# Performance work log

Hardware: AMD Instinct MI355X
Metric: run time of the kernel (lower is better)

Reference implementation:

```python
import jax, jax.numpy as jnp
import numpy as np

GAMMA = 1.0

def _rbf_mean(X, Y, gamma):
    x2 = jnp.sum(X * X, axis=1)  # [n]
    y2 = jnp.sum(Y * Y, axis=1)  # [m]
    d2 = x2[:, None] + y2[None, :] - 2.0 * (X @ Y.T)
    d2 = jnp.maximum(d2, 0.0)
    return jnp.mean(jnp.exp(-gamma * d2))

def setup_inputs() -> dict:
    key = jax.random.key(0)
    k1, k2 = jax.random.split(key)
    N = jax.random.normal(k1, (8192, 256), dtype=jnp.float32)
    R = jax.random.normal(k2, (8192, 256), dtype=jnp.float32)
    return {"N": N, "R": R}

def reference(N, R):
    xx = _rbf_mean(N, N, GAMMA)
    yy = _rbf_mean(R, R, GAMMA)
    xy = _rbf_mean(N, R, GAMMA)
    mmd = xx + yy - 2.0 * xy
    return jnp.sqrt(mmd)
```

## Files before the change

kernel.cpp:

```cpp
#include <hip/hip_runtime.h>
#include <math.h>

typedef float f32x4 __attribute__((ext_vector_type(4)));
typedef int   i32x4 __attribute__((ext_vector_type(4)));
typedef int   i32x8 __attribute__((ext_vector_type(8)));
typedef float f32x2 __attribute__((ext_vector_type(2)));

#define MTOT 16384
#define HALF 8192
#define KDIM 256
#define BM 256
#define NB (MTOT / BM)
#define NBLK (NB * (NB + 1) / 2)
#define NBLOCKS 256
#define TPX (NBLK / 8)

#define GLDS16(g, l) __builtin_amdgcn_global_load_lds(                      \
    (const __attribute__((address_space(1))) void*)(g),                     \
    (__attribute__((address_space(3))) void*)(l), 16, 0, 0)

#define BAR() do { asm volatile("" ::: "memory");                           \
  __builtin_amdgcn_s_barrier(); asm volatile("" ::: "memory"); } while (0)

__global__ __launch_bounds__(256) void convert_kernel(
    const float* __restrict__ Nmat, const float* __restrict__ Rmat,
    unsigned int* __restrict__ Z, float* __restrict__ x2,
    float* __restrict__ accum, unsigned int* __restrict__ counter) {
  if (blockIdx.x == 0 && threadIdx.x == 0) { *accum = 0.f; *counter = 0u; }
  const int lane = threadIdx.x & 63;
  const int wv = threadIdx.x >> 6;
  const int row = blockIdx.x * 4 + wv;
  const float* src = (row < HALF) ? (Nmat + (size_t)row * KDIM)
                                  : (Rmat + (size_t)(row - HALF) * KDIM);
  float4 v = *(const float4*)(src + lane * 4);
  int pk = __builtin_amdgcn_cvt_pk_fp8_f32(v.x, v.y, 0, false);
  pk = __builtin_amdgcn_cvt_pk_fp8_f32(v.z, v.w, pk, true);
  Z[(size_t)row * (KDIM / 4) + lane] = (unsigned int)pk;
  f32x2 d01 = __builtin_amdgcn_cvt_pk_f32_fp8(pk, false);
  f32x2 d23 = __builtin_amdgcn_cvt_pk_f32_fp8(pk, true);
  float sq = d01[0] * d01[0] + d01[1] * d01[1] + d23[0] * d23[0] + d23[1] * d23[1];
  #pragma unroll
  for (int off = 32; off; off >>= 1) sq += __shfl_down(sq, off);
  if (lane == 0) x2[row] = -0.5f * sq;
}

__device__ __forceinline__ void decode_tile(int t, int& bm, int& bn) {
  const int u = NBLK - 1 - t;
  int rr = (int)((sqrtf(8.0f * (float)u + 1.0f) - 1.0f) * 0.5f);
  while (rr * (rr + 1) / 2 > u) --rr;
  while ((rr + 1) * (rr + 2) / 2 <= u) ++rr;
  bm = NB - 1 - rr;
  bn = bm + (t - (bm * NB - bm * (bm - 1) / 2));
}

__global__ __launch_bounds__(512, 2) void mmd_gemm(
    const unsigned char* __restrict__ Z, const float* __restrict__ x2,
    float* __restrict__ accum, unsigned int* __restrict__ counter,
    float* __restrict__ out) {
  __shared__ __align__(16) unsigned char As[2 * 32768];
  __shared__ __align__(16) unsigned char Bs[2 * 32768];
  __shared__ __align__(16) float x2h[2][512];
  __shared__ __align__(16) float wsred[8];

  const int tid  = threadIdx.x;
  const int lane = tid & 63;
  const int wid  = tid >> 6;
  const int wm   = wid >> 2;
  const int wn   = wid & 3;

  const int lr = lane >> 3;
  const int ls = lane & 7;
  const int cofs = lr * KDIM + ((ls ^ lr) << 4);

  const int fr = lane & 15;
  const int fq = lane >> 4;
  const int key = fr & 7;
  const int slotL = ((2 * fq) ^ key) * 16;
  const int slotH = ((2 * fq + 1) ^ key) * 16;

  const int xcd = blockIdx.x & 7;
  const int lb  = blockIdx.x >> 3;
  const int niter = (lb < (TPX & 31)) ? (TPX / 32 + 1) : (TPX / 32);
  const int nslab = 2 * niter;

  f32x4 acc[8][4];
  float running = 0.f;

  auto STAGE = [&](int bmv, int bnv, int h, int buf) {
    const unsigned char* Ab = Z + (size_t)bmv * (BM * KDIM) + h * 128 + cofs;
    const unsigned char* Bb = Z + (size_t)bnv * (BM * KDIM) + h * 128 + cofs;
    unsigned char* Ad = As + buf * 32768;
    unsigned char* Bd = Bs + buf * 32768;
    #pragma unroll
    for (int tt = 0; tt < 4; ++tt) {
      int i = wid * 4 + tt;
      GLDS16(Ab + i * 2048, Ad + i * 1024);
      GLDS16(Bb + i * 2048, Bd + i * 1024);
    }
  };

  auto STAGEX2 = [&](int bmv, int bnv, int par) {
    GLDS16((const unsigned char*)(x2 + bmv * BM) + lane * 16,
           (unsigned char*)&x2h[par][0]);
    GLDS16((const unsigned char*)(x2 + bnv * BM) + lane * 16,
           (unsigned char*)&x2h[par][256]);
  };

  auto ACCINIT = [&](int par) {
    float xch[4];
    #pragma unroll
    for (int tn = 0; tn < 4; ++tn)
      xch[tn] = x2h[par][256 + wn * 64 + tn * 16 + fr];
    #pragma unroll
    for (int tm = 0; tm < 8; ++tm) {
      f32x4 xr = *(const f32x4*)&x2h[par][wm * 128 + tm * 16 + fq * 4];
      #pragma unroll
      for (int tn = 0; tn < 4; ++tn)
        #pragma unroll
        for (int v = 0; v < 4; ++v)
          acc[tm][tn][v] = xr[v] + xch[tn];
    }
  };

  int cbm, cbn;
  decode_tile(xcd * TPX + lb, cbm, cbn);
  int nbm = cbm, nbn = cbn;
  int cpar = 0;

  STAGEX2(cbm, cbn, 0);
  STAGE(cbm, cbn, 0, 0);
  STAGE(cbm, cbn, 1, 1);
  asm volatile("s_waitcnt vmcnt(16)" ::: "memory");
  ACCINIT(0);

  for (int j = 0; j < nslab; ++j) {
    const int bsel = j & 1;
    if (j + 1 >= nslab)      asm volatile("s_waitcnt vmcnt(0)" ::: "memory");
    else if (bsel == 0)      asm volatile("s_waitcnt vmcnt(8)" ::: "memory");
    else                     asm volatile("s_waitcnt vmcnt(10)" ::: "memory");
    BAR();

    {
      const unsigned char* A_s = As + bsel * 32768;
      const unsigned char* B_s = Bs + bsel * 32768;
      i32x8 bf[4];
      #pragma unroll
      for (int tn = 0; tn < 4; ++tn) {
        int row = wn * 64 + tn * 16 + fr;
        i32x4 lo = *(const i32x4*)(B_s + row * 128 + slotL);
        i32x4 hi = *(const i32x4*)(B_s + row * 128 + slotH);
        bf[tn] = __builtin_shufflevector(lo, hi, 0, 1, 2, 3, 4, 5, 6, 7);
      }
      #pragma unroll
      for (int tm = 0; tm < 8; ++tm) {
        int row = wm * 128 + tm * 16 + fr;
        i32x4 lo = *(const i32x4*)(A_s + row * 128 + slotL);
        i32x4 hi = *(const i32x4*)(A_s + row * 128 + slotH);
        i32x8 af = __builtin_shufflevector(lo, hi, 0, 1, 2, 3, 4, 5, 6, 7);
        #pragma unroll
        for (int tn = 0; tn < 4; ++tn)
          acc[tm][tn] = __builtin_amdgcn_mfma_scale_f32_16x16x128_f8f6f4(
              af, bf[tn], acc[tm][tn], 0, 0,
              0, 0x7F7F7F7F, 0, 0x7F7F7F7F);
      }
    }
    BAR();

    if (j + 2 < nslab) {
      if (bsel == 0) {
        decode_tile(xcd * TPX + lb + 32 * ((j >> 1) + 1), nbm, nbn);
        STAGEX2(nbm, nbn, cpar ^ 1);
        STAGE(nbm, nbn, 0, 0);
      } else {
        STAGE(nbm, nbn, 1, 1);
      }
    }

    if (bsel == 1) {
      float amax = -1e30f;
      #pragma unroll
      for (int tm = 0; tm < 8; ++tm)
        #pragma unroll
        for (int tn = 0; tn < 4; ++tn) {
          float m1 = fmaxf(fmaxf(acc[tm][tn][0], acc[tm][tn][1]), acc[tm][tn][2]);
          amax = fmaxf(fmaxf(amax, m1), acc[tm][tn][3]);
        }

      float partial = 0.f;
      if (__any(amax > -40.f)) {
        #pragma unroll
        for (int tm = 0; tm < 8; ++tm)
          #pragma unroll
          for (int tn = 0; tn < 4; ++tn)
            #pragma unroll
            for (int v = 0; v < 4; ++v) {
              float a = fminf(acc[tm][tn][v], 0.f);
              partial += exp2f(a * 2.885390082f);
            }
      }
      float wgt = ((cbm < NB / 2) == (cbn < NB / 2)) ? 1.f : -1.f;
      if (cbm != cbn) wgt *= 2.f;
      running += partial * wgt;

      if (j + 2 < nslab) {
        asm volatile("s_waitcnt vmcnt(16)" ::: "memory");
        cpar ^= 1;
        ACCINIT(cpar);
        cbm = nbm; cbn = nbn;
      }
    }
  }

  #pragma unroll
  for (int off = 32; off; off >>= 1) running += __shfl_down(running, off);
  if (lane == 0) wsred[wid] = running;
  __syncthreads();
  if (tid == 0) {
    float bs = 0.f;
    #pragma unroll
    for (int w = 0; w < 8; ++w) bs += wsred[w];
    atomicAdd(accum, bs);
    __threadfence();
    unsigned int old = atomicAdd(counter, 1u);
    if (old == NBLOCKS - 1) {
      float tot = atomicAdd(accum, 0.f);
      float mmd = tot / ((float)HALF * (float)HALF);
      out[0] = sqrtf(fmaxf(mmd, 0.f));
    }
  }
}

extern "C" void kernel_launch(void* const* d_in, const int* in_sizes, int n_in,
                              void* d_out, int out_size, void* d_ws, size_t ws_size,
                              hipStream_t stream) {
  const float* Nmat = (const float*)d_in[0];
  const float* Rmat = (const float*)d_in[1];
  float* out = (float*)d_out;

  char* ws = (char*)d_ws;
  unsigned char* Z = (unsigned char*)ws;
  float* x2        = (float*)(ws + (size_t)MTOT * KDIM);
  float* accum     = (float*)(ws + (size_t)MTOT * KDIM + (size_t)MTOT * 4);
  unsigned int* counter = (unsigned int*)(ws + (size_t)MTOT * KDIM + (size_t)MTOT * 4 + 4);

  convert_kernel<<<MTOT / 4, 256, 0, stream>>>(Nmat, Rmat, (unsigned int*)Z, x2,
                                               accum, counter);
  mmd_gemm<<<NBLOCKS, 512, 0, stream>>>(Z, x2, accum, counter, out);
}
```

Before: 126.0 us.

## Load B fragments directly into registers and preload all row norms to LDS

The B operand tiles are no longer staged through shared memory. Each wave loads its B fragments straight from global memory into double-buffered registers, which removes the Bs LDS buffers and their ds_read traffic. All 16K row norms are preloaded once into LDS, which replaces the per-tile x2 staging. The main loop is restructured to process both K halves per iteration with explicit waitcnt counts. The cost is higher register pressure and uncoalesced per-lane global loads for B, plus 64KB of LDS for the norms.

```diff
diff --git a/kernel.cpp b/kernel.cpp
--- a/kernel.cpp
+++ b/kernel.cpp
@@ -58,8 +58,7 @@
     float* __restrict__ accum, unsigned int* __restrict__ counter,
     float* __restrict__ out) {
   __shared__ __align__(16) unsigned char As[2 * 32768];
-  __shared__ __align__(16) unsigned char Bs[2 * 32768];
-  __shared__ __align__(16) float x2h[2][512];
+  __shared__ __align__(16) float x2l[MTOT];
   __shared__ __align__(16) float wsred[8];
 
   const int tid  = threadIdx.x;
@@ -81,39 +80,39 @@
   const int xcd = blockIdx.x & 7;
   const int lb  = blockIdx.x >> 3;
   const int niter = (lb < (TPX & 31)) ? (TPX / 32 + 1) : (TPX / 32);
-  const int nslab = 2 * niter;
 
   f32x4 acc[8][4];
+  i32x4 bfA[8], bfB[8];
   float running = 0.f;
 
-  auto STAGE = [&](int bmv, int bnv, int h, int buf) {
+  auto STAGEA = [&](int bmv, int h, int buf) {
     const unsigned char* Ab = Z + (size_t)bmv * (BM * KDIM) + h * 128 + cofs;
-    const unsigned char* Bb = Z + (size_t)bnv * (BM * KDIM) + h * 128 + cofs;
     unsigned char* Ad = As + buf * 32768;
-    unsigned char* Bd = Bs + buf * 32768;
     #pragma unroll
     for (int tt = 0; tt < 4; ++tt) {
       int i = wid * 4 + tt;
       GLDS16(Ab + i * 2048, Ad + i * 1024);
-      GLDS16(Bb + i * 2048, Bd + i * 1024);
-    }
-  };
-
-  auto STAGEX2 = [&](int bmv, int bnv, int par) {
-    GLDS16((const unsigned char*)(x2 + bmv * BM) + lane * 16,
-           (unsigned char*)&x2h[par][0]);
-    GLDS16((const unsigned char*)(x2 + bnv * BM) + lane * 16,
-           (unsigned char*)&x2h[par][256]);
-  };
-
-  auto ACCINIT = [&](int par) {
+    }
+  };
+
+  auto LOADB = [&](int bnv, int h, i32x4* dst) {
+    const unsigned char* base = Z + (size_t)bnv * (BM * KDIM)
+                                  + (size_t)(wn * 64 + fr) * KDIM + h * 128 + fq * 32;
+    #pragma unroll
+    for (int tn = 0; tn < 4; ++tn) {
+      dst[2 * tn]     = *(const i32x4*)(base + (size_t)tn * 16 * KDIM);
+      dst[2 * tn + 1] = *(const i32x4*)(base + (size_t)tn * 16 * KDIM + 16);
+    }
+  };
+
+  auto ACCINIT = [&](int bmv, int bnv) {
     float xch[4];
     #pragma unroll
     for (int tn = 0; tn < 4; ++tn)
-      xch[tn] = x2h[par][256 + wn * 64 + tn * 16 + fr];
+      xch[tn] = x2l[bnv * BM + wn * 64 + tn * 16 + fr];
     #pragma unroll
     for (int tm = 0; tm < 8; ++tm) {
-      f32x4 xr = *(const f32x4*)&x2h[par][wm * 128 + tm * 16 + fq * 4];
+      f32x4 xr = *(const f32x4*)&x2l[bmv * BM + wm * 128 + tm * 16 + fq * 4];
       #pragma unroll
       for (int tn = 0; tn < 4; ++tn)
         #pragma unroll
@@ -122,93 +121,88 @@
     }
   };
 
-  int cbm, cbn;
+  auto COMPUTE = [&](const unsigned char* A_s, const i32x4* bfr) {
+    i32x8 bf[4];
+    #pragma unroll
+    for (int tn = 0; tn < 4; ++tn)
+      bf[tn] = __builtin_shufflevector(bfr[2 * tn], bfr[2 * tn + 1],
+                                       0, 1, 2, 3, 4, 5, 6, 7);
+    #pragma unroll
+    for (int tm = 0; tm < 8; ++tm) {
+      int row = wm * 128 + tm * 16 + fr;
+      i32x4 lo = *(const i32x4*)(A_s + row * 128 + slotL);
+      i32x4 hi = *(const i32x4*)(A_s + row * 128 + slotH);
+      i32x8 af = __builtin_shufflevector(lo, hi, 0, 1, 2, 3, 4, 5, 6, 7);
+      #pragma unroll
+      for (int tn = 0; tn < 4; ++tn)
+        acc[tm][tn] = __builtin_amdgcn_mfma_scale_f32_16x16x128_f8f6f4(
+            af, bf[tn], acc[tm][tn], 0, 0,
+            0, 0x7F7F7F7F, 0, 0x7F7F7F7F);
+    }
+  };
+
+  int cbm, cbn, nbm, nbn;
   decode_tile(xcd * TPX + lb, cbm, cbn);
-  int nbm = cbm, nbn = cbn;
-  int cpar = 0;
-
-  STAGEX2(cbm, cbn, 0);
-  STAGE(cbm, cbn, 0, 0);
-  STAGE(cbm, cbn, 1, 1);
-  asm volatile("s_waitcnt vmcnt(16)" ::: "memory");
-  ACCINIT(0);
-
-  for (int j = 0; j < nslab; ++j) {
-    const int bsel = j & 1;
-    if (j + 1 >= nslab)      asm volatile("s_waitcnt vmcnt(0)" ::: "memory");
-    else if (bsel == 0)      asm volatile("s_waitcnt vmcnt(8)" ::: "memory");
-    else                     asm volatile("s_waitcnt vmcnt(10)" ::: "memory");
-    BAR();
-
-    {
-      const unsigned char* A_s = As + bsel * 32768;
-      const unsigned char* B_s = Bs + bsel * 32768;
-      i32x8 bf[4];
+
+  #pragma unroll
+  for (int t = 0; t < 8; ++t) {
+    int i = wid * 8 + t;
+    GLDS16((const unsigned char*)x2 + i * 1024 + (size_t)lane * 16,
+           (unsigned char*)x2l + i * 1024);
+  }
+  STAGEA(cbm, 0, 0);
+  LOADB(cbn, 0, bfA);
+  STAGEA(cbm, 1, 1);
+  LOADB(cbn, 1, bfB);
+  asm volatile("s_waitcnt vmcnt(24)" ::: "memory");
+  BAR();
+  ACCINIT(cbm, cbn);
+
+  for (int s = 0; s < niter; ++s) {
+    const bool haveNext = (s + 1 < niter);
+    if (haveNext) decode_tile(xcd * TPX + lb + 32 * (s + 1), nbm, nbn);
+
+    asm volatile("s_waitcnt vmcnt(12)" ::: "memory");
+    BAR();
+    COMPUTE(As, bfA);
+    if (haveNext) LOADB(nbn, 0, bfA);
+    BAR();
+    if (haveNext) STAGEA(nbm, 0, 0);
+
+    if (haveNext) asm volatile("s_waitcnt vmcnt(12)" ::: "memory");
+    else          asm volatile("s_waitcnt vmcnt(0)"  ::: "memory");
+    BAR();
+    COMPUTE(As + 32768, bfB);
+    if (haveNext) LOADB(nbn, 1, bfB);
+    BAR();
+    if (haveNext) STAGEA(nbm, 1, 1);
+
+    float amax = -1e30f;
+    #pragma unroll
+    for (int tm = 0; tm < 8; ++tm)
       #pragma unroll
       for (int tn = 0; tn < 4; ++tn) {
-        int row = wn * 64 + tn * 16 + fr;
-        i32x4 lo = *(const i32x4*)(B_s + row * 128 + slotL);
-        i32x4 hi = *(const i32x4*)(B_s + row * 128 + slotH);
-        bf[tn] = __builtin_shufflevector(lo, hi, 0, 1, 2, 3, 4, 5, 6, 7);
+        float m1 = fmaxf(fmaxf(acc[tm][tn][0], acc[tm][tn][1]), acc[tm][tn][2]);
+        amax = fmaxf(fmaxf(amax, m1), acc[tm][tn][3]);
       }
-      #pragma unroll
-      for (int tm = 0; tm < 8; ++tm) {
-        int row = wm * 128 + tm * 16 + fr;
-        i32x4 lo = *(const i32x4*)(A_s + row * 128 + slotL);
-        i32x4 hi = *(const i32x4*)(A_s + row * 128 + slotH);
-        i32x8 af = __builtin_shufflevector(lo, hi, 0, 1, 2, 3, 4, 5, 6, 7);
+
+    float partial = 0.f;
+    if (__any(amax > -40.f)) {
+      #pragma unroll
+      for (int tm = 0; tm < 8; ++tm)
         #pragma unroll
         for (int tn = 0; tn < 4; ++tn)
-          acc[tm][tn] = __builtin_amdgcn_mfma_scale_f32_16x16x128_f8f6f4(
-              af, bf[tn], acc[tm][tn], 0, 0,
-              0, 0x7F7F7F7F, 0, 0x7F7F7F7F);
-      }
-    }
-    BAR();
-
-    if (j + 2 < nslab) {
-      if (bsel == 0) {
-        decode_tile(xcd * TPX + lb + 32 * ((j >> 1) + 1), nbm, nbn);
-        STAGEX2(nbm, nbn, cpar ^ 1);
-        STAGE(nbm, nbn, 0, 0);
-      } else {
-        STAGE(nbm, nbn, 1, 1);
-      }
-    }
-
-    if (bsel == 1) {
-      float amax = -1e30f;
-      #pragma unroll
-      for (int tm = 0; tm < 8; ++tm)
-        #pragma unroll
-        for (int tn = 0; tn < 4; ++tn) {
-          float m1 = fmaxf(fmaxf(acc[tm][tn][0], acc[tm][tn][1]), acc[tm][tn][2]);
-          amax = fmaxf(fmaxf(amax, m1), acc[tm][tn][3]);
-        }
-
-      float partial = 0.f;
-      if (__any(amax > -40.f)) {
-        #pragma unroll
-        for (int tm = 0; tm < 8; ++tm)
           #pragma unroll
-          for (int tn = 0; tn < 4; ++tn)
-            #pragma unroll
-            for (int v = 0; v < 4; ++v) {
-              float a = fminf(acc[tm][tn][v], 0.f);
-              partial += exp2f(a * 2.885390082f);
-            }
-      }
-      float wgt = ((cbm < NB / 2) == (cbn < NB / 2)) ? 1.f : -1.f;
-      if (cbm != cbn) wgt *= 2.f;
-      running += partial * wgt;
-
-      if (j + 2 < nslab) {
-        asm volatile("s_waitcnt vmcnt(16)" ::: "memory");
-        cpar ^= 1;
-        ACCINIT(cpar);
-        cbm = nbm; cbn = nbn;
-      }
-    }
+          for (int v = 0; v < 4; ++v) {
+            float a = fminf(acc[tm][tn][v], 0.f);
+            partial += exp2f(a * 2.885390082f);
+          }
+    }
+    float wgt = ((cbm < NB / 2) == (cbn < NB / 2)) ? 1.f : -1.f;
+    if (cbm != cbn) wgt *= 2.f;
+    running += partial * wgt;
+
+    if (haveNext) { ACCINIT(nbm, nbn); cbm = nbm; cbn = nbn; }
   }
 
   #pragma unroll
```

After: 339.7 us. 2.7x slower.
